# Kernel tuning notes

Measured on AMD Instinct MI355X. Metric: run time of the kernel, lower is better.

The kernel has to match this reference:

```python
import jax, jax.numpy as jnp
import numpy as np

HEADS = 8

def setup_inputs() -> dict:
    key = jax.random.key(0)
    ks = jax.random.split(key, 4)
    b, n, d = 4, 4097, 128  # n = 64*64 + 1 (CLS + spatial)
    x = jax.random.normal(ks[0], (b, n, d), dtype=jnp.float32)
    W_qkv = jax.random.normal(ks[1], (d, 3 * d), dtype=jnp.float32) * (d ** -0.5)
    b_qkv = jnp.zeros((3 * d,), dtype=jnp.float32)
    W_out = jax.random.normal(ks[2], (d, d), dtype=jnp.float32) * (d ** -0.5)
    b_out = jnp.zeros((d,), dtype=jnp.float32)
    return {"x": x, "W_qkv": W_qkv, "b_qkv": b_qkv, "W_out": W_out, "b_out": b_out}

def reference(x, W_qkv, b_qkv, W_out, b_out):
    b, n, d = x.shape
    h = HEADS
    dh = d // h
    scale = d ** -0.5  # note: module scales by dim**-0.5, not head_dim**-0.5
    qkv = x @ W_qkv + b_qkv                      # [b, n, 3d]
    q, k, v = jnp.split(qkv, 3, axis=-1)
    def to_heads(t):
        return t.reshape(b, n, h, dh).transpose(0, 2, 1, 3)  # [b, h, n, dh]
    q, k, v = to_heads(q), to_heads(k), to_heads(v)
    dots = jnp.einsum('bhid,bhjd->bhij', q, k) * scale       # [b, h, n, n]
    attn = jax.nn.softmax(dots, axis=-1)
    out = jnp.einsum('bhij,bhjd->bhid', attn, v)             # [b, h, n, dh]
    out = out.transpose(0, 2, 1, 3).reshape(b, n, d)
    return out @ W_out + b_out
```

## Files before the change

kernel.cpp:

```cpp
#include <hip/hip_runtime.h>
#include <hip/hip_bf16.h>
#include <stdint.h>


#define BB 4
#define NN 4097
#define NNP 4112
#define DD 128
#define HH 8
#define DH 16
#define BH (BB*HH)
#define ROWS (BB*NN)
#define MT  1025

typedef _Float16 h4 __attribute__((ext_vector_type(4)));
typedef _Float16 h8 __attribute__((ext_vector_type(8)));
typedef __fp16   fp16v2 __attribute__((ext_vector_type(2)));
typedef float    f4 __attribute__((ext_vector_type(4)));

#define QSCALE (0.08838834764831845f * 1.4426950408889634f)

#if __has_builtin(__builtin_amdgcn_exp2f)
#define EXP2F(x) __builtin_amdgcn_exp2f(x)
#else
#define EXP2F(x) exp2f(x)
#endif

union H4u { h4 v; fp16v2 p[2]; };

static __device__ __forceinline__ H4u pack4u(float a, float b, float c, float d) {
    H4u u;
#if __has_builtin(__builtin_amdgcn_cvt_pkrtz)
    u.p[0] = __builtin_amdgcn_cvt_pkrtz(a, b);
    u.p[1] = __builtin_amdgcn_cvt_pkrtz(c, d);
#else
    u.v[0] = (_Float16)a; u.v[1] = (_Float16)b; u.v[2] = (_Float16)c; u.v[3] = (_Float16)d;
#endif
    return u;
}

__global__ __launch_bounds__(256) void prep(
    const float* __restrict__ x,
    const float* __restrict__ Wqkv,
    const float* __restrict__ Wout,
    _Float16* __restrict__ x16,
    _Float16* __restrict__ WqkvT,
    _Float16* __restrict__ WoutT)
{
    const int id = blockIdx.x*256 + threadIdx.x;
    const int NX8 = ROWS*DD/8;
    if (id < NX8) {
        const float4* s = (const float4*)(x + (size_t)id*8);
        const float4 a = s[0], b = s[1];
        const H4u u0 = pack4u(a.x, a.y, a.z, a.w);
        const H4u u1 = pack4u(b.x, b.y, b.z, b.w);
        h4* d = (h4*)(x16 + (size_t)id*8);
        d[0] = u0.v; d[1] = u1.v;
    } else if (id < NX8 + 384*128) {
        const int e = id - NX8;
        const int n = e >> 7, k = e & 127;
        const float s = (n < 128) ? QSCALE : 1.0f;
        WqkvT[e] = (_Float16)(Wqkv[k*384 + n] * s);
    } else if (id < NX8 + 384*128 + 128*128) {
        const int e = id - NX8 - 384*128;
        const int n = e >> 7, k = e & 127;
        WoutT[e] = (_Float16)(Wout[k*128 + n]);
    }
}

__global__ __launch_bounds__(256) void qkv_mfma(
    const _Float16* __restrict__ x16,
    const _Float16* __restrict__ WqkvT,
    const float* __restrict__ bqkv,
    _Float16* __restrict__ Qh,
    _Float16* __restrict__ Kh,
    _Float16* __restrict__ Vh)
{
    const int wid  = blockIdx.x*4 + (threadIdx.x >> 6);
    if (wid >= MT) return;
    const int lane = threadIdx.x & 63;
    const int quad = lane >> 4, l16 = lane & 15;

    const int arow = wid*16 + l16;
    const int arc  = (arow < ROWS) ? arow : (ROWS - 1);
    h4 af[8];
    #pragma unroll
    for (int kk = 0; kk < 8; ++kk)
        af[kk] = *(const h4*)(x16 + (size_t)arc*DD + kk*16 + quad*4);

    const int r0 = wid*16 + quad*4;

    for (int nt = 0; nt < 24; nt += 2) {
        const float b0 = bqkv[nt*16 + l16]      * ((nt   < 8) ? QSCALE : 1.0f);
        const float b1 = bqkv[nt*16 + 16 + l16] * ((nt+1 < 8) ? QSCALE : 1.0f);
        f4 a0 = {b0,b0,b0,b0}, a1 = {b1,b1,b1,b1};
        #pragma unroll
        for (int kk = 0; kk < 8; ++kk) {
            const h4 bf0 = *(const h4*)(WqkvT + (size_t)(nt*16     + l16)*DD + kk*16 + quad*4);
            const h4 bf1 = *(const h4*)(WqkvT + (size_t)(nt*16 + 16 + l16)*DD + kk*16 + quad*4);
            a0 = __builtin_amdgcn_mfma_f32_16x16x16f16(af[kk], bf0, a0, 0, 0, 0);
            a1 = __builtin_amdgcn_mfma_f32_16x16x16f16(af[kk], bf1, a1, 0, 0, 0);
        }
        #pragma unroll
        for (int u = 0; u < 2; ++u) {
            const int ntc = nt + u;
            const int which = ntc >> 3, head = ntc & 7;
            _Float16* base = (which == 0) ? Qh : ((which == 1) ? Kh : Vh);
            const f4 av = u ? a1 : a0;
            #pragma unroll
            for (int r = 0; r < 4; ++r) {
                const int row = r0 + r;
                if (row < ROWS) {
                    const int bidx = row / NN;
                    const int nrow = row - bidx*NN;
                    base[((size_t)(bidx*HH + head)*NNP + nrow)*DH + l16] = (_Float16)av[r];
                }
            }
        }
    }
}

__global__ __launch_bounds__(256) void vt_transpose(
    const _Float16* __restrict__ Vh,
    _Float16* __restrict__ Vt)
{
    __shared__ _Float16 tile[128][DH + 2];
    const int tl  = blockIdx.x;
    const int bh  = blockIdx.y;
    const int tid = threadIdx.x;
    const int n0  = tl * 128;
    const int rem = (n0 + 128 <= NNP) ? 128 : (NNP - n0);

    {
        const int r  = tid >> 1;
        const int i8 = (tid & 1) * 8;
        const int rc = (r < rem) ? r : (rem - 1);
        const h8 v = *(const h8*)(Vh + ((size_t)bh*NNP + n0 + rc)*DH + i8);
        #pragma unroll
        for (int j = 0; j < 8; ++j) tile[r][i8 + j] = v[j];
    }
    __syncthreads();
    {
        const int i    = tid >> 4;
        const int nseg = tid & 15;
        if (nseg * 8 < rem) {
            h8 v;
            #pragma unroll
            for (int j = 0; j < 8; ++j) v[j] = tile[nseg*8 + j][i];
            *(h8*)(Vt + ((size_t)bh*DH + i)*NNP + n0 + nseg*8) = v;
        }
    }
}

__global__ __launch_bounds__(256, 8) void attn_mfma(
    const _Float16* __restrict__ Qh,
    const _Float16* __restrict__ Kh,
    const _Float16* __restrict__ Vt,
    _Float16* __restrict__ PACC,
    float* __restrict__ PL)
{
    const int qt   = blockIdx.x;
    const int bh   = blockIdx.y;
    const int sp   = blockIdx.z;
    const int tid  = threadIdx.x;
    const int wave = tid >> 6;
    const int lane = tid & 63;
    const int quad = lane >> 4;
    const int l16  = lane & 15;
    const int bidx = bh >> 3, head = bh & 7;

    const int qbase = qt*256 + wave*64;

    const _Float16* Qb = Qh + (size_t)bh*NNP*DH;
    h4 qf[4];
    #pragma unroll
    for (int g = 0; g < 4; ++g) {
        const int qr = qbase + g*16 + l16;
        const int qc = (qr < NN) ? qr : (NN-1);
        qf[g] = *(const h4*)(Qb + (size_t)qc*DH + quad*4);
    }

    f4 acc[4] = {{0,0,0,0},{0,0,0,0},{0,0,0,0},{0,0,0,0}};
    float ls[4] = {0.f,0.f,0.f,0.f};

    const int t0 = sp*64;
    const int t1 = t0 + 64;

    const _Float16* kp = Kh + ((size_t)bh*NNP + (size_t)t0*16 + l16)*DH + quad*4;
    const _Float16* vp = Vt + ((size_t)bh*DH + l16)*NNP + t0*16 + quad*4;

    h4 ak = *(const h4*)kp;
    h4 av = *(const h4*)vp;
    const f4 zero = {0.f,0.f,0.f,0.f};
#if __has_builtin(__builtin_amdgcn_fdot2)
    const fp16v2 one2 = {(__fp16)1.0f, (__fp16)1.0f};
#endif

    for (int tt = t0; tt < t1; ++tt) {
        kp += 16*DH; vp += 16;
        const h4 nak = *(const h4*)kp;
        const h4 nav = *(const h4*)vp;
        #pragma unroll
        for (int g = 0; g < 4; ++g) {
            f4 d = __builtin_amdgcn_mfma_f32_16x16x16f16(ak, qf[g], zero, 0, 0, 0);
            const float p0 = EXP2F(d[0]), p1 = EXP2F(d[1]), p2 = EXP2F(d[2]), p3 = EXP2F(d[3]);
            const H4u pb = pack4u(p0, p1, p2, p3);
#if __has_builtin(__builtin_amdgcn_fdot2)
            ls[g] = __builtin_amdgcn_fdot2(pb.p[0], one2,
                     __builtin_amdgcn_fdot2(pb.p[1], one2, ls[g], false), false);
#else
            ls[g] += (p0 + p1) + (p2 + p3);
#endif
            acc[g] = __builtin_amdgcn_mfma_f32_16x16x16f16(av, pb.v, acc[g], 0, 0, 0);
        }
        ak = nak; av = nav;
    }

    if (sp == 3) {
        #pragma unroll
        for (int g = 0; g < 4; ++g) {
            f4 d = __builtin_amdgcn_mfma_f32_16x16x16f16(ak, qf[g], zero, 0, 0, 0);
            const float p0 = (quad == 0) ? EXP2F(d[0]) : 0.f;
            ls[g] += p0;
            const H4u pb = pack4u(p0, 0.f, 0.f, 0.f);
            acc[g] = __builtin_amdgcn_mfma_f32_16x16x16f16(av, pb.v, acc[g], 0, 0, 0);
        }
    }

    const size_t rb = (size_t)sp*ROWS + (size_t)bidx*NN;
    #pragma unroll
    for (int g = 0; g < 4; ++g) {
        float l = ls[g];
        l += __shfl_xor(l, 16);
        l += __shfl_xor(l, 32);
        const int qr = qbase + g*16 + l16;
        if (qr < NN) {
            const float inv = 1.0f / l;
            const H4u st = pack4u(acc[g][0]*inv, acc[g][1]*inv, acc[g][2]*inv, acc[g][3]*inv);
            *(h4*)(PACC + (rb + qr)*DD + head*DH + quad*4) = st.v;
            if (quad == 0) PL[(rb + qr)*HH + head] = l;
        }
    }
}

__global__ __launch_bounds__(256) void out_mfma(
    const _Float16* __restrict__ PACC,
    const float* __restrict__ PL,
    const _Float16* __restrict__ WoutT,
    const float* __restrict__ bout,
    float* __restrict__ out)
{
    const int wid  = blockIdx.x*4 + (threadIdx.x >> 6);
    if (wid >= MT) return;
    const int lane = threadIdx.x & 63;
    const int quad = lane >> 4, l16 = lane & 15;

    const int arow = wid*16 + l16;
    const int arc  = (arow < ROWS) ? arow : (ROWS - 1);

    h4 af[8];
    #pragma unroll
    for (int kk = 0; kk < 8; ++kk) {
        float n0 = 0.f, n1 = 0.f, n2 = 0.f, n3 = 0.f, lsum = 0.f;
        #pragma unroll
        for (int sp = 0; sp < 4; ++sp) {
            const float l = PL[((size_t)sp*ROWS + arc)*HH + kk];
            lsum += l;
            const h4 p = *(const h4*)(PACC + ((size_t)sp*ROWS + arc)*DD + kk*16 + quad*4);
            n0 += l*(float)p[0]; n1 += l*(float)p[1];
            n2 += l*(float)p[2]; n3 += l*(float)p[3];
        }
        const float inv = 1.0f / lsum;
        const H4u u = pack4u(n0*inv, n1*inv, n2*inv, n3*inv);
        af[kk] = u.v;
    }

    const int r0 = wid*16 + quad*4;

    for (int nt = 0; nt < 8; nt += 2) {
        const float b0 = bout[nt*16 + l16];
        const float b1 = bout[nt*16 + 16 + l16];
        f4 a0 = {b0,b0,b0,b0}, a1 = {b1,b1,b1,b1};
        #pragma unroll
        for (int kk = 0; kk < 8; ++kk) {
            const h4 bf0 = *(const h4*)(WoutT + (size_t)(nt*16      + l16)*DD + kk*16 + quad*4);
            const h4 bf1 = *(const h4*)(WoutT + (size_t)(nt*16 + 16 + l16)*DD + kk*16 + quad*4);
            a0 = __builtin_amdgcn_mfma_f32_16x16x16f16(af[kk], bf0, a0, 0, 0, 0);
            a1 = __builtin_amdgcn_mfma_f32_16x16x16f16(af[kk], bf1, a1, 0, 0, 0);
        }
        #pragma unroll
        for (int r = 0; r < 4; ++r) {
            const int row = r0 + r;
            if (row < ROWS) {
                out[(size_t)row*DD + nt*16      + l16] = a0[r];
                out[(size_t)row*DD + nt*16 + 16 + l16] = a1[r];
            }
        }
    }
}

extern "C" void kernel_launch(void* const* d_in, const int* in_sizes, int n_in,
                              void* d_out, int out_size, void* d_ws, size_t ws_size,
                              hipStream_t stream) {
    const float* x    = (const float*)d_in[0];
    const float* Wqkv = (const float*)d_in[1];
    const float* bqkv = (const float*)d_in[2];
    const float* Wout = (const float*)d_in[3];
    const float* bout = (const float*)d_in[4];
    for (int i = 0; i < n_in; ++i) {
        switch (in_sizes[i]) {
            case 2097664: x    = (const float*)d_in[i]; break;
            case 49152:   Wqkv = (const float*)d_in[i]; break;
            case 384:     bqkv = (const float*)d_in[i]; break;
            case 16384:   Wout = (const float*)d_in[i]; break;
            case 128:     bout = (const float*)d_in[i]; break;
            default: break;
        }
    }
    float* out = (float*)d_out;

    const size_t perh = (size_t)BH * NNP * DH;
    _Float16* Qh   = (_Float16*)d_ws;
    _Float16* Kh   = Qh + perh;
    _Float16* Vt   = Kh + perh;
    _Float16* Vh   = Vt + perh;
    _Float16* PACC = Vh;
    _Float16* x16  = Vh + perh;
    float*    PL    = (float*)(PACC + (size_t)4*ROWS*DD);
    _Float16* WqkvT = (_Float16*)(PL + (size_t)4*ROWS*HH);
    _Float16* WoutT = WqkvT + 384*128;

    const int NX8 = ROWS*DD/8;
    const int prep_total = NX8 + 384*128 + 128*128;

    hipLaunchKernelGGL(prep, dim3((prep_total + 255)/256), dim3(256), 0, stream,
                       x, Wqkv, Wout, x16, WqkvT, WoutT);
    hipLaunchKernelGGL(qkv_mfma, dim3((MT + 3)/4), dim3(256), 0, stream,
                       x16, WqkvT, bqkv, Qh, Kh, Vh);
    hipLaunchKernelGGL(vt_transpose, dim3(33, BH), dim3(256), 0, stream,
                       Vh, Vt);
    hipLaunchKernelGGL(attn_mfma, dim3(17, BH, 4), dim3(256), 0, stream,
                       Qh, Kh, Vt, PACC, PL);
    hipLaunchKernelGGL(out_mfma, dim3((MT + 3)/4), dim3(256), 0, stream,
                       PACC, PL, WoutT, bout, out);
}
```

Measured before the change: 196.8 us.

## Fuse x conversion into QKV GEMM, split N across waves, MFMA row sums

Removes the separate fp32-to-fp16 conversion of x by converting inside the QKV projection. The QKV and output projections now give each block one 16-row tile and split the output columns across its four waves, which launches more blocks. In attention, the softmax row sums come from an extra MFMA against a ones vector instead of fdot2 plus cross-lane shuffles, and the occupancy hint drops from 8 to 4. The extra MFMA doubles matrix-core work per PV step, and each of the four waves in a projection block reloads the same x rows.

Result: slower. 223.2 us (+13.4%).

```diff
diff --git a/kernel.cpp b/kernel.cpp
--- a/kernel.cpp
+++ b/kernel.cpp
@@ -40,57 +40,50 @@
 }
 
 __global__ __launch_bounds__(256) void prep(
-    const float* __restrict__ x,
     const float* __restrict__ Wqkv,
     const float* __restrict__ Wout,
-    _Float16* __restrict__ x16,
     _Float16* __restrict__ WqkvT,
     _Float16* __restrict__ WoutT)
 {
     const int id = blockIdx.x*256 + threadIdx.x;
-    const int NX8 = ROWS*DD/8;
-    if (id < NX8) {
-        const float4* s = (const float4*)(x + (size_t)id*8);
-        const float4 a = s[0], b = s[1];
-        const H4u u0 = pack4u(a.x, a.y, a.z, a.w);
-        const H4u u1 = pack4u(b.x, b.y, b.z, b.w);
-        h4* d = (h4*)(x16 + (size_t)id*8);
-        d[0] = u0.v; d[1] = u1.v;
-    } else if (id < NX8 + 384*128) {
-        const int e = id - NX8;
-        const int n = e >> 7, k = e & 127;
+    if (id < 384*128) {
+        const int n = id >> 7, k = id & 127;
         const float s = (n < 128) ? QSCALE : 1.0f;
-        WqkvT[e] = (_Float16)(Wqkv[k*384 + n] * s);
-    } else if (id < NX8 + 384*128 + 128*128) {
-        const int e = id - NX8 - 384*128;
+        WqkvT[id] = (_Float16)(Wqkv[k*384 + n] * s);
+    } else if (id < 384*128 + 128*128) {
+        const int e = id - 384*128;
         const int n = e >> 7, k = e & 127;
         WoutT[e] = (_Float16)(Wout[k*128 + n]);
     }
 }
 
 __global__ __launch_bounds__(256) void qkv_mfma(
-    const _Float16* __restrict__ x16,
+    const float* __restrict__ x,
     const _Float16* __restrict__ WqkvT,
     const float* __restrict__ bqkv,
     _Float16* __restrict__ Qh,
     _Float16* __restrict__ Kh,
     _Float16* __restrict__ Vh)
 {
-    const int wid  = blockIdx.x*4 + (threadIdx.x >> 6);
-    if (wid >= MT) return;
+    const int wid  = blockIdx.x;
+    const int wave = threadIdx.x >> 6;
     const int lane = threadIdx.x & 63;
     const int quad = lane >> 4, l16 = lane & 15;
 
     const int arow = wid*16 + l16;
     const int arc  = (arow < ROWS) ? arow : (ROWS - 1);
+    const float* xr = x + (size_t)arc*DD;
     h4 af[8];
     #pragma unroll
-    for (int kk = 0; kk < 8; ++kk)
-        af[kk] = *(const h4*)(x16 + (size_t)arc*DD + kk*16 + quad*4);
+    for (int kk = 0; kk < 8; ++kk) {
+        const float4 t = *(const float4*)(xr + kk*16 + quad*4);
+        af[kk] = pack4u(t.x, t.y, t.z, t.w).v;
+    }
 
     const int r0 = wid*16 + quad*4;
-
-    for (int nt = 0; nt < 24; nt += 2) {
+    const int nt0 = wave*6;
+
+    for (int nt = nt0; nt < nt0 + 6; nt += 2) {
         const float b0 = bqkv[nt*16 + l16]      * ((nt   < 8) ? QSCALE : 1.0f);
         const float b1 = bqkv[nt*16 + 16 + l16] * ((nt+1 < 8) ? QSCALE : 1.0f);
         f4 a0 = {b0,b0,b0,b0}, a1 = {b1,b1,b1,b1};
@@ -152,7 +145,7 @@
     }
 }
 
-__global__ __launch_bounds__(256, 8) void attn_mfma(
+__global__ __launch_bounds__(256, 4) void attn_mfma(
     const _Float16* __restrict__ Qh,
     const _Float16* __restrict__ Kh,
     const _Float16* __restrict__ Vt,
@@ -180,8 +173,9 @@
         qf[g] = *(const h4*)(Qb + (size_t)qc*DH + quad*4);
     }
 
-    f4 acc[4] = {{0,0,0,0},{0,0,0,0},{0,0,0,0},{0,0,0,0}};
-    float ls[4] = {0.f,0.f,0.f,0.f};
+    f4 acc[4]  = {{0,0,0,0},{0,0,0,0},{0,0,0,0},{0,0,0,0}};
+    f4 lacc[4] = {{0,0,0,0},{0,0,0,0},{0,0,0,0},{0,0,0,0}};
+    const h4 ones4 = {(_Float16)1.f, (_Float16)1.f, (_Float16)1.f, (_Float16)1.f};
 
     const int t0 = sp*64;
     const int t1 = t0 + 64;
@@ -192,9 +186,6 @@
     h4 ak = *(const h4*)kp;
     h4 av = *(const h4*)vp;
     const f4 zero = {0.f,0.f,0.f,0.f};
-#if __has_builtin(__builtin_amdgcn_fdot2)
-    const fp16v2 one2 = {(__fp16)1.0f, (__fp16)1.0f};
-#endif
 
     for (int tt = t0; tt < t1; ++tt) {
         kp += 16*DH; vp += 16;
@@ -205,13 +196,8 @@
             f4 d = __builtin_amdgcn_mfma_f32_16x16x16f16(ak, qf[g], zero, 0, 0, 0);
             const float p0 = EXP2F(d[0]), p1 = EXP2F(d[1]), p2 = EXP2F(d[2]), p3 = EXP2F(d[3]);
             const H4u pb = pack4u(p0, p1, p2, p3);
-#if __has_builtin(__builtin_amdgcn_fdot2)
-            ls[g] = __builtin_amdgcn_fdot2(pb.p[0], one2,
-                     __builtin_amdgcn_fdot2(pb.p[1], one2, ls[g], false), false);
-#else
-            ls[g] += (p0 + p1) + (p2 + p3);
-#endif
-            acc[g] = __builtin_amdgcn_mfma_f32_16x16x16f16(av, pb.v, acc[g], 0, 0, 0);
+            lacc[g] = __builtin_amdgcn_mfma_f32_16x16x16f16(ones4, pb.v, lacc[g], 0, 0, 0);
+            acc[g]  = __builtin_amdgcn_mfma_f32_16x16x16f16(av,    pb.v, acc[g],  0, 0, 0);
         }
         ak = nak; av = nav;
     }
@@ -221,18 +207,16 @@
         for (int g = 0; g < 4; ++g) {
             f4 d = __builtin_amdgcn_mfma_f32_16x16x16f16(ak, qf[g], zero, 0, 0, 0);
             const float p0 = (quad == 0) ? EXP2F(d[0]) : 0.f;
-            ls[g] += p0;
             const H4u pb = pack4u(p0, 0.f, 0.f, 0.f);
-            acc[g] = __builtin_amdgcn_mfma_f32_16x16x16f16(av, pb.v, acc[g], 0, 0, 0);
+            lacc[g] = __builtin_amdgcn_mfma_f32_16x16x16f16(ones4, pb.v, lacc[g], 0, 0, 0);
+            acc[g]  = __builtin_amdgcn_mfma_f32_16x16x16f16(av,    pb.v, acc[g],  0, 0, 0);
         }
     }
 
     const size_t rb = (size_t)sp*ROWS + (size_t)bidx*NN;
     #pragma unroll
     for (int g = 0; g < 4; ++g) {
-        float l = ls[g];
-        l += __shfl_xor(l, 16);
-        l += __shfl_xor(l, 32);
+        const float l = lacc[g][0];
         const int qr = qbase + g*16 + l16;
         if (qr < NN) {
             const float inv = 1.0f / l;
@@ -250,8 +234,8 @@
     const float* __restrict__ bout,
     float* __restrict__ out)
 {
-    const int wid  = blockIdx.x*4 + (threadIdx.x >> 6);
-    if (wid >= MT) return;
+    const int wid  = blockIdx.x;
+    const int wave = threadIdx.x >> 6;
     const int lane = threadIdx.x & 63;
     const int quad = lane >> 4, l16 = lane & 15;
 
@@ -276,8 +260,9 @@
     }
 
     const int r0 = wid*16 + quad*4;
-
-    for (int nt = 0; nt < 8; nt += 2) {
+    const int nt = wave*2;
+
+    {
         const float b0 = bout[nt*16 + l16];
         const float b1 = bout[nt*16 + 16 + l16];
         f4 a0 = {b0,b0,b0,b0}, a1 = {b1,b1,b1,b1};
@@ -325,22 +310,20 @@
     _Float16* Vt   = Kh + perh;
     _Float16* Vh   = Vt + perh;
     _Float16* PACC = Vh;
-    _Float16* x16  = Vh + perh;
     float*    PL    = (float*)(PACC + (size_t)4*ROWS*DD);
     _Float16* WqkvT = (_Float16*)(PL + (size_t)4*ROWS*HH);
     _Float16* WoutT = WqkvT + 384*128;
 
-    const int NX8 = ROWS*DD/8;
-    const int prep_total = NX8 + 384*128 + 128*128;
+    const int prep_total = 384*128 + 128*128;
 
     hipLaunchKernelGGL(prep, dim3((prep_total + 255)/256), dim3(256), 0, stream,
-                       x, Wqkv, Wout, x16, WqkvT, WoutT);
-    hipLaunchKernelGGL(qkv_mfma, dim3((MT + 3)/4), dim3(256), 0, stream,
-                       x16, WqkvT, bqkv, Qh, Kh, Vh);
+                       Wqkv, Wout, WqkvT, WoutT);
+    hipLaunchKernelGGL(qkv_mfma, dim3(MT), dim3(256), 0, stream,
+                       x, WqkvT, bqkv, Qh, Kh, Vh);
     hipLaunchKernelGGL(vt_transpose, dim3(33, BH), dim3(256), 0, stream,
                        Vh, Vt);
     hipLaunchKernelGGL(attn_mfma, dim3(17, BH, 4), dim3(256), 0, stream,
                        Qh, Kh, Vt, PACC, PL);
-    hipLaunchKernelGGL(out_mfma, dim3((MT + 3)/4), dim3(256), 0, stream,
+    hipLaunchKernelGGL(out_mfma, dim3(MT), dim3(256), 0, stream,
                        PACC, PL, WoutT, bout, out);
 }
```
